# Kernel optimization log

Measured on AMD Instinct MI355X. Metric: run time of the kernel, lower is better.

## Reference

```python
import jax, jax.numpy as jnp
import numpy as np

TILE = 128  # hardcoded tile size in tile_cache/untile_cache


def setup_inputs() -> dict:
    key = jax.random.key(0)
    k1, k2 = jax.random.split(key)
    B, H, D, T = 4, 8, 128, 64  # max_len = TILE * T = 8192
    # K stored tiled-transposed: (B, H, D, 128, num_tiles)
    k_cache = jax.random.normal(k1, (B, H, D, TILE, T), dtype=jnp.float32)
    # V stored tiled: (B, H, 128, num_tiles, D)
    v_cache = jax.random.normal(k2, (B, H, TILE, T, D), dtype=jnp.float32)
    return {"k_cache": k_cache, "v_cache": v_cache, "seq_len": 6144}


def reference(k_cache, v_cache, seq_len):
    # untile_cache, transposed=True: (B,H,D,128,T) -> (B,H,D,128*T)  [BHDS]
    B, H, D, tile, T = k_cache.shape
    k = k_cache.reshape(B, H, D, tile * T)
    # untile_cache, transposed=False: (B,H,128,T,D) -> (B,H,128*T,D)  [BHSD]
    Bv, Hv, tile_v, Tv, Dv = v_cache.shape
    v = v_cache.reshape(Bv, Hv, tile_v * Tv, Dv)
    # _slice_kv_cacheline, padding_side='right': slice [0, seq_len) on seq dim
    k = k[:, :, :, :seq_len]        # seq dim = 3 (transposed K)
    v = v[:, :, :seq_len, :]        # seq dim = 2
    # stack into a single output: transpose K back to BHSD to match V layout
    k_bhsd = jnp.swapaxes(k, 2, 3)  # (B,H,S,D)
    return jnp.stack([k_bhsd, v], axis=0)  # (2, B, H, seq_len, D)
```

## Files before the change

kernel.cpp:

```cpp
#include <hip/hip_runtime.h>


#define BH 32
#define DD 128

typedef float f4 __attribute__((ext_vector_type(4)));

__device__ __forceinline__ void gload_lds16(const float* g, float* l) {
    __builtin_amdgcn_global_load_lds(
        (const __attribute__((address_space(1))) void*)g,
        (__attribute__((address_space(3))) void*)l,
        16, 0, 0);
}

__global__ __launch_bounds__(256) void kv_repack(
    const float* __restrict__ kc, const float* __restrict__ vc,
    float* __restrict__ out,
    int S, int Sfull, int kBlocks, int vBlocksPerBH, int f4PerVBlock)
{
    __shared__ float lds[64 * DD];

    const int bid = blockIdx.x;
    const int t = threadIdx.x;

    if (bid < kBlocks) {
        const int sTiles = S >> 7;
        const int perBH  = 2 * sTiles;
        const int bh     = bid / perBH;
        const int rem    = bid - bh * perBH;
        const int dTile  = rem / sTiles;
        const int sTile  = rem - dTile * sTiles;

        const int wave = t >> 6;
        const int lane = t & 63;

        {
            const float* rowbase = kc
                + (size_t)(bh * DD + dTile * 64) * (size_t)Sfull
                + (size_t)(sTile << 7);
            const int c  = lane & 31;
            const int dh = lane >> 5;
#pragma unroll
            for (int i = 0; i < 8; ++i) {
                const int dbase = (wave << 4) + (i << 1);
                const int d  = dbase + dh;
                const int s4 = c ^ (d >> 2);
                gload_lds16(rowbase + (size_t)d * Sfull + (s4 << 2),
                            &lds[dbase << 7]);
            }
        }
        __syncthreads();

        {
            const int d4 = t & 15;
            const int r0 = t >> 4;
            float* dstBase = out
                + ((size_t)bh * S + (size_t)(sTile << 7)) * DD
                + dTile * 64 + (d4 << 2);
#pragma unroll
            for (int i = 0; i < 8; ++i) {
                const int sr  = (i << 4) + r0;
                const int col = (((sr >> 2) ^ d4) << 2) + (sr & 3);
                const int base = (d4 << 9) + col;
                f4 v;
                v.x = lds[base];
                v.y = lds[base + DD];
                v.z = lds[base + 2 * DD];
                v.w = lds[base + 3 * DD];
                __builtin_nontemporal_store(v, (f4*)(dstBase + (size_t)sr * DD));
            }
        }
    } else {
        const int vb   = bid - kBlocks;
        const int bh   = vb / vBlocksPerBH;
        const int part = vb - bh * vBlocksPerBH;

        const size_t f4PerBHsrc = (size_t)Sfull * (DD / 4);
        const size_t f4PerBHdst = (size_t)S * (DD / 4);
        const size_t outVOff    = (size_t)BH * S * (DD / 4);

        const f4* src = (const f4*)vc + (size_t)bh * f4PerBHsrc
                        + (size_t)part * f4PerVBlock;
        f4* dst = (f4*)out + outVOff + (size_t)bh * f4PerBHdst
                  + (size_t)part * f4PerVBlock;

        const int n = f4PerVBlock;
        int j = t;
        for (; j + 768 < n; j += 1024) {
            f4 a0 = __builtin_nontemporal_load(src + j);
            f4 a1 = __builtin_nontemporal_load(src + j + 256);
            f4 a2 = __builtin_nontemporal_load(src + j + 512);
            f4 a3 = __builtin_nontemporal_load(src + j + 768);
            __builtin_nontemporal_store(a0, dst + j);
            __builtin_nontemporal_store(a1, dst + j + 256);
            __builtin_nontemporal_store(a2, dst + j + 512);
            __builtin_nontemporal_store(a3, dst + j + 768);
        }
        for (; j < n; j += 256) {
            f4 a = __builtin_nontemporal_load(src + j);
            __builtin_nontemporal_store(a, dst + j);
        }
    }
}

extern "C" void kernel_launch(void* const* d_in, const int* in_sizes, int n_in,
                              void* d_out, int out_size, void* d_ws, size_t ws_size,
                              hipStream_t stream) {
    const float* kc = (const float*)d_in[0];
    const float* vc = (const float*)d_in[1];
    float* out = (float*)d_out;

    const int S     = out_size / (2 * BH * DD);
    const int Sfull = in_sizes[0] / (BH * DD);

    const int sTiles        = S >> 7;
    const int kBlocks       = BH * 2 * sTiles;
    const int vBlocksPerBH  = sTiles;
    const int f4PerVBlock   = (S * (DD / 4)) / vBlocksPerBH;
    const int vBlocks       = BH * vBlocksPerBH;

    dim3 grid(kBlocks + vBlocks);
    dim3 block(256);
    kv_repack<<<grid, block, 0, stream>>>(kc, vc, out, S, Sfull,
                                          kBlocks, vBlocksPerBH, f4PerVBlock);
}
```

Before: 353.9 us.

## Retile K transpose to full-D by 64-seq tiles and interleave K/V blocks

Each K block now transposes all 128 D rows for a 64-wide sequence slice instead of 64 D rows for a 128-wide slice. Each output row segment is then written as a full contiguous 512-byte row, and the LDS swizzle is adjusted to the new tile shape. The grid is also interleaved so every third block is a V copy block, mixing K transposes with V streaming copies across the machine instead of running all K blocks first. Global reads per K row become 256 bytes instead of 512, which may reduce read burst efficiency.

```diff
diff --git a/kernel.cpp b/kernel.cpp
--- a/kernel.cpp
+++ b/kernel.cpp
@@ -16,62 +16,61 @@
 __global__ __launch_bounds__(256) void kv_repack(
     const float* __restrict__ kc, const float* __restrict__ vc,
     float* __restrict__ out,
-    int S, int Sfull, int kBlocks, int vBlocksPerBH, int f4PerVBlock)
+    int S, int Sfull, int sTiles, int vBlocksPerBH, int f4PerVBlock)
 {
-    __shared__ float lds[64 * DD];
+    __shared__ float lds[128 * 64];
 
     const int bid = blockIdx.x;
     const int t = threadIdx.x;
+    const int r3 = bid % 3;
 
-    if (bid < kBlocks) {
-        const int sTiles = S >> 7;
-        const int perBH  = 2 * sTiles;
-        const int bh     = bid / perBH;
-        const int rem    = bid - bh * perBH;
-        const int dTile  = rem / sTiles;
-        const int sTile  = rem - dTile * sTiles;
+    if (r3 != 2) {
+        const int kb    = (bid / 3) * 2 + r3;
+        const int bh    = kb / sTiles;
+        const int sTile = kb - bh * sTiles;
 
         const int wave = t >> 6;
         const int lane = t & 63;
 
         {
+            const int c  = lane & 15;
+            const int dh = lane >> 4;
             const float* rowbase = kc
-                + (size_t)(bh * DD + dTile * 64) * (size_t)Sfull
-                + (size_t)(sTile << 7);
-            const int c  = lane & 31;
-            const int dh = lane >> 5;
+                + (size_t)(bh * DD) * (size_t)Sfull
+                + (size_t)(sTile << 6);
 #pragma unroll
             for (int i = 0; i < 8; ++i) {
-                const int dbase = (wave << 4) + (i << 1);
+                const int dbase = (wave << 5) + (i << 2);
                 const int d  = dbase + dh;
-                const int s4 = c ^ (d >> 2);
+                const int s4 = c ^ ((d >> 2) & 7);
                 gload_lds16(rowbase + (size_t)d * Sfull + (s4 << 2),
-                            &lds[dbase << 7]);
+                            &lds[dbase << 6]);
             }
         }
         __syncthreads();
 
         {
-            const int d4 = t & 15;
-            const int r0 = t >> 4;
+            const int d4 = t & 31;
+            const int r0 = t >> 5;
+            const int swz = d4 & 7;
             float* dstBase = out
-                + ((size_t)bh * S + (size_t)(sTile << 7)) * DD
-                + dTile * 64 + (d4 << 2);
+                + ((size_t)bh * S + (size_t)(sTile << 6)) * DD
+                + (d4 << 2);
 #pragma unroll
             for (int i = 0; i < 8; ++i) {
-                const int sr  = (i << 4) + r0;
-                const int col = (((sr >> 2) ^ d4) << 2) + (sr & 3);
-                const int base = (d4 << 9) + col;
+                const int sr   = (i << 3) + r0;
+                const int base = (d4 << 8)
+                               + ((((sr >> 2) ^ swz) << 2) + (sr & 3));
                 f4 v;
                 v.x = lds[base];
-                v.y = lds[base + DD];
-                v.z = lds[base + 2 * DD];
-                v.w = lds[base + 3 * DD];
+                v.y = lds[base + 64];
+                v.z = lds[base + 128];
+                v.w = lds[base + 192];
                 __builtin_nontemporal_store(v, (f4*)(dstBase + (size_t)sr * DD));
             }
         }
     } else {
-        const int vb   = bid - kBlocks;
+        const int vb   = bid / 3;
         const int bh   = vb / vBlocksPerBH;
         const int part = vb - bh * vBlocksPerBH;
 
@@ -113,14 +112,14 @@
     const int S     = out_size / (2 * BH * DD);
     const int Sfull = in_sizes[0] / (BH * DD);
 
-    const int sTiles        = S >> 7;
-    const int kBlocks       = BH * 2 * sTiles;
-    const int vBlocksPerBH  = sTiles;
+    const int sTiles        = S >> 6;
+    const int kBlocks       = BH * sTiles;
+    const int vBlocksPerBH  = S >> 7;
     const int f4PerVBlock   = (S * (DD / 4)) / vBlocksPerBH;
     const int vBlocks       = BH * vBlocksPerBH;
 
     dim3 grid(kBlocks + vBlocks);
     dim3 block(256);
     kv_repack<<<grid, block, 0, stream>>>(kc, vc, out, S, Sfull,
-                                          kBlocks, vBlocksPerBH, f4PerVBlock);
+                                          sTiles, vBlocksPerBH, f4PerVBlock);
 }
```

New measurement: 361.1 us. 1.02x slower.
